# Kernel tuning notes

Hardware: AMD Instinct MI355X
Metric: run time of the kernel (lower is better)

## Reference

```python
import jax, jax.numpy as jnp
import numpy as np

D, E, H, B, K = 2, 16, 1024, 8192, 2  # depth, experts, width, tokens, selection_size


def setup_inputs() -> dict:
    key = jax.random.key(0)
    ks = jax.random.split(key, 6)
    X = jax.random.normal(ks[0], (B, H), dtype=jnp.float32)
    # gate Linear per layer (torch inits these to zero; small random used so top-k is nontrivial)
    gate_w = jax.random.normal(ks[1], (D, E, H), dtype=jnp.float32) * 0.02
    gate_b = jnp.zeros((D, E), dtype=jnp.float32)
    # per-expert Linear: weight [out,in], bias [out], stacked over (layer, expert)
    ew = jax.random.normal(ks[2], (D, E, H, H), dtype=jnp.float32) * (1.0 / np.float32(np.sqrt(H)))
    eb = jnp.zeros((D, E, H), dtype=jnp.float32)
    # PReLU params: left/right slopes ~ randn (as in torch init), position/bias zero
    pl = jax.random.normal(ks[3], (D, E, H), dtype=jnp.float32)
    pr = jax.random.normal(ks[4], (D, E, H), dtype=jnp.float32)
    pp = jnp.zeros((D, E, H), dtype=jnp.float32)
    pb = jnp.zeros((D, E, H), dtype=jnp.float32)
    return {"X": X, "gate_w": gate_w, "gate_b": gate_b, "ew": ew, "eb": eb,
            "pl": pl, "pr": pr, "pp": pp, "pb": pb}


def reference(X, gate_w, gate_b, ew, eb, pl, pr, pp, pb):
    x = X
    for d in range(D):  # small fixed layer loop
        # gating: Linear -> top-k -> softmax over selected logits
        G = jnp.einsum('bi,ei->be', x, gate_w[d]) + gate_b[d]          # [B,E]
        vals, idx = jax.lax.top_k(G, K)                                 # [B,K]
        w = jax.nn.softmax(vals, axis=-1)                               # [B,K]
        # expert Linear over all experts, then custom PReLU
        y = jnp.einsum('bi,eoi->beo', x, ew[d]) + eb[d]                 # [B,E,O]
        delta = y - pp[d]                                               # [B,E,O]
        act = pb[d] + jnp.where(delta >= 0, delta * pr[d], delta * pl[d])
        # gather selected experts and combine
        sel = jnp.take_along_axis(act, idx[:, :, None], axis=1)        # [B,K,O]
        x = jnp.einsum('bk,bko->bo', w, sel)                            # [B,O]
    return x
```

## Files before the change

### kernel.cpp

```cpp
#include <hip/hip_runtime.h>

#define H_ 1024
#define B_ 8192
#define E_ 16
#define D_ 2
#define BM 128
#define BN 128
#define BK 32
#define MAXT 144

typedef _Float16 f16;
typedef _Float16 f16x4 __attribute__((ext_vector_type(4)));
typedef _Float16 f16x8 __attribute__((ext_vector_type(8)));
typedef float    f32x4 __attribute__((ext_vector_type(4)));

__device__ __forceinline__ void gload16(const void* g, void* l) {
  __builtin_amdgcn_global_load_lds((const __attribute__((address_space(1))) void*)g,
                                   (__attribute__((address_space(3))) void*)l, 16, 0, 0);
}

__global__ void split_kernel(const float* __restrict__ s, f16* __restrict__ hp,
                             f16* __restrict__ lp, int n) {
  const int stride = gridDim.x * blockDim.x * 4;
  for (int i = (blockIdx.x * blockDim.x + threadIdx.x) * 4; i < n; i += stride) {
    float4 v = *(const float4*)(s + i);
    f16 h0 = (f16)v.x, h1 = (f16)v.y, h2 = (f16)v.z, h3 = (f16)v.w;
    f16 l0 = (f16)(v.x - (float)h0), l1 = (f16)(v.y - (float)h1);
    f16 l2 = (f16)(v.z - (float)h2), l3 = (f16)(v.w - (float)h3);
    *(f16x4*)(hp + i) = (f16x4){h0, h1, h2, h3};
    *(f16x4*)(lp + i) = (f16x4){l0, l1, l2, l3};
  }
}

__global__ void gate_split(const float* __restrict__ x, const float* __restrict__ gw,
                           const float* __restrict__ gb, f16* __restrict__ xh,
                           f16* __restrict__ xl, int2* __restrict__ tok_e,
                           float2* __restrict__ tok_w) {
  const int token = blockIdx.x * 4 + (threadIdx.x >> 6);
  const int lane = threadIdx.x & 63;
  const float4* xr = (const float4*)(x + (long)token * H_);
  f16x4* hr = (f16x4*)(xh + (long)token * H_);
  f16x4* lr = (f16x4*)(xl + (long)token * H_);
  float acc[E_];
#pragma unroll
  for (int e = 0; e < E_; ++e) acc[e] = 0.f;
#pragma unroll
  for (int i0 = 0; i0 < H_ / 4; i0 += 64) {
    float4 xv = xr[i0 + lane];
    f16 h0 = (f16)xv.x, h1 = (f16)xv.y, h2 = (f16)xv.z, h3 = (f16)xv.w;
    hr[i0 + lane] = (f16x4){h0, h1, h2, h3};
    lr[i0 + lane] = (f16x4){(f16)(xv.x - (float)h0), (f16)(xv.y - (float)h1),
                            (f16)(xv.z - (float)h2), (f16)(xv.w - (float)h3)};
#pragma unroll
    for (int e = 0; e < E_; ++e) {
      float4 gv = ((const float4*)(gw + e * H_))[i0 + lane];
      acc[e] = fmaf(xv.x, gv.x, fmaf(xv.y, gv.y, fmaf(xv.z, gv.z, fmaf(xv.w, gv.w, acc[e]))));
    }
  }
#pragma unroll
  for (int off = 32; off; off >>= 1) {
#pragma unroll
    for (int e = 0; e < E_; ++e) acc[e] += __shfl_xor(acc[e], off, 64);
  }
  if (lane == 0) {
    float g[E_];
#pragma unroll
    for (int e = 0; e < E_; ++e) g[e] = acc[e] + gb[e];
    int i0 = 0; float v0 = g[0];
#pragma unroll
    for (int e = 1; e < E_; ++e) if (g[e] > v0) { v0 = g[e]; i0 = e; }
    int i1 = -1; float v1 = -3.4e38f;
#pragma unroll
    for (int e = 0; e < E_; ++e) if (e != i0 && g[e] > v1) { v1 = g[e]; i1 = e; }
    float t = expf(v1 - v0);
    float s = 1.f / (1.f + t);
    tok_e[token] = (int2){i0, i1};
    tok_w[token] = (float2){s, t * s};
  }
}

__global__ void route_kernel(const int2* __restrict__ tok_e, const float2* __restrict__ tok_w,
                             int* __restrict__ lists, float* __restrict__ wlist,
                             int* __restrict__ counts) {
  __shared__ int cnt[E_];
  __shared__ int base[E_];
  const int tid = threadIdx.x;
  const int token = blockIdx.x * 256 + tid;
  if (tid < E_) cnt[tid] = 0;
  __syncthreads();
  int2 e = tok_e[token];
  float2 w = tok_w[token];
  int p0 = atomicAdd(&cnt[e.x], 1);
  int p1 = atomicAdd(&cnt[e.y], 1);
  __syncthreads();
  if (tid < E_) base[tid] = atomicAdd(&counts[tid], cnt[tid]);
  __syncthreads();
  int o0 = e.x * B_ + base[e.x] + p0;
  lists[o0] = token; wlist[o0] = w.x;
  int o1 = e.y * B_ + base[e.y] + p1;
  lists[o1] = token; wlist[o1] = w.y;
}

__global__ void build_tiles(const int* __restrict__ counts, int2* __restrict__ tiles,
                            int* __restrict__ ntile) {
  if (threadIdx.x == 0) {
    int n = 0;
    for (int e = 0; e < E_; ++e) {
      int c = counts[e];
      for (int mt = 0; mt * BM < c; ++mt) tiles[n++] = (int2){e, mt};
    }
    *ntile = n;
  }
}

__global__ __launch_bounds__(256, 4) void expert_gemm(
    const f16* __restrict__ xh, const f16* __restrict__ xl,
    const f16* __restrict__ wh, const f16* __restrict__ wl,
    const float* __restrict__ eb, const float* __restrict__ pl,
    const float* __restrict__ pr, const float* __restrict__ pp,
    const float* __restrict__ pb, const int* __restrict__ lists,
    const float* __restrict__ wlist, const int* __restrict__ counts,
    const int2* __restrict__ tiles, const int* __restrict__ ntile,
    float* __restrict__ out) {
  const int t = blockIdx.y;
  if (t >= *ntile) return;
  const int2 td = tiles[t];
  const int e = td.x, mt = td.y;
  const int cnt = counts[e];
  const int nt = blockIdx.x;

  __shared__ char smem[32768];

  const int tid = threadIdx.x;
  const int lane = tid & 63;
  const int wave = tid >> 6;
  const int wm = wave >> 1, wn = wave & 1;

  const int rl = lane >> 2;
  const int ks = ((lane & 3) - ((lane >> 3) & 3)) & 3;
  const int c0 = wave * 2, c1 = wave * 2 + 1;
  const int rA0 = c0 * 16 + rl, rA1 = c1 * 16 + rl;
  const int gr0 = mt * BM + rA0, gr1 = mt * BM + rA1;
  const int tok0 = (gr0 < cnt) ? lists[e * B_ + gr0] : 0;
  const int tok1 = (gr1 < cnt) ? lists[e * B_ + gr1] : 0;
  const long a0 = (long)tok0 * H_ + ks * 8;
  const long a1 = (long)tok1 * H_ + ks * 8;
  const long b0 = ((long)e * H_ + nt * BN + rA0) * H_ + ks * 8;
  const long b1 = ((long)e * H_ + nt * BN + rA1) * H_ + ks * 8;

  const int rm = lane & 15;
  const int sl = ((((lane >> 4) + (rm >> 1)) & 3) << 4);
  int offA[4], offB[4];
#pragma unroll
  for (int m = 0; m < 4; ++m) offA[m] = (wm * 64 + m * 16 + rm) * 64 + sl;
#pragma unroll
  for (int n = 0; n < 4; ++n) offB[n] = (wn * 64 + n * 16 + rm) * 64 + sl;

  f32x4 acc[4][4] = {};

  for (int kt = 0; kt < H_; kt += BK) {
    gload16(xh + a0 + kt, smem + c0 * 1024);
    gload16(xh + a1 + kt, smem + c1 * 1024);
    gload16(xl + a0 + kt, smem + 8192 + c0 * 1024);
    gload16(xl + a1 + kt, smem + 8192 + c1 * 1024);
    gload16(wh + b0 + kt, smem + 16384 + c0 * 1024);
    gload16(wh + b1 + kt, smem + 16384 + c1 * 1024);
    gload16(wl + b0 + kt, smem + 24576 + c0 * 1024);
    gload16(wl + b1 + kt, smem + 24576 + c1 * 1024);
    __syncthreads();

    f16x8 Amh[4], Aml[4], Bnh[4], Bnl[4];
#pragma unroll
    for (int m = 0; m < 4; ++m) {
      Amh[m] = *(const f16x8*)(smem + offA[m]);
      Aml[m] = *(const f16x8*)(smem + 8192 + offA[m]);
    }
#pragma unroll
    for (int n = 0; n < 4; ++n) {
      Bnh[n] = *(const f16x8*)(smem + 16384 + offB[n]);
      Bnl[n] = *(const f16x8*)(smem + 24576 + offB[n]);
    }
#pragma unroll
    for (int m = 0; m < 4; ++m) {
#pragma unroll
      for (int n = 0; n < 4; ++n) {
        acc[m][n] = __builtin_amdgcn_mfma_f32_16x16x32_f16(Amh[m], Bnh[n], acc[m][n], 0, 0, 0);
        acc[m][n] = __builtin_amdgcn_mfma_f32_16x16x32_f16(Amh[m], Bnl[n], acc[m][n], 0, 0, 0);
        acc[m][n] = __builtin_amdgcn_mfma_f32_16x16x32_f16(Aml[m], Bnh[n], acc[m][n], 0, 0, 0);
      }
    }
    __syncthreads();
  }

  float ebv[4], plv[4], prv[4], ppv[4], pbv[4];
  int Ocol[4];
#pragma unroll
  for (int n = 0; n < 4; ++n) {
    int O = nt * BN + wn * 64 + n * 16 + rm;
    Ocol[n] = O;
    int idx = e * H_ + O;
    ebv[n] = eb[idx]; plv[n] = pl[idx]; prv[n] = pr[idx]; ppv[n] = pp[idx]; pbv[n] = pb[idx];
  }
  const int rbase = (lane >> 4) * 4;
#pragma unroll
  for (int m = 0; m < 4; ++m) {
#pragma unroll
    for (int j = 0; j < 4; ++j) {
      int rloc = wm * 64 + m * 16 + rbase + j;
      int gr = mt * BM + rloc;
      if (gr < cnt) {
        float wgt = wlist[e * B_ + gr];
        long obase = (long)lists[e * B_ + gr] * H_;
#pragma unroll
        for (int n = 0; n < 4; ++n) {
          float y = acc[m][n][j] + ebv[n];
          float dlt = y - ppv[n];
          float act = pbv[n] + (dlt >= 0.f ? dlt * prv[n] : dlt * plv[n]);
          atomicAdd(out + obase + Ocol[n], wgt * act);
        }
      }
    }
  }
}

extern "C" void kernel_launch(void* const* d_in, const int* in_sizes, int n_in,
                              void* d_out, int out_size, void* d_ws, size_t ws_size,
                              hipStream_t stream) {
  const float* X  = (const float*)d_in[0];
  const float* GW = (const float*)d_in[1];
  const float* GB = (const float*)d_in[2];
  const float* EW = (const float*)d_in[3];
  const float* EB = (const float*)d_in[4];
  const float* PL = (const float*)d_in[5];
  const float* PR = (const float*)d_in[6];
  const float* PP = (const float*)d_in[7];
  const float* PB = (const float*)d_in[8];
  float* out = (float*)d_out;

  char* ws = (char*)d_ws;
  float* x1    = (float*)(ws);
  f16*   xh    = (f16*)(ws + 33554432);
  f16*   xl    = (f16*)(ws + 50331648);
  f16*   wh    = (f16*)(ws + 67108864);
  f16*   wl    = (f16*)(ws + 100663296);
  int*   lists = (int*)(ws + 134217728);
  float* wlist = (float*)(ws + 134742016);
  int*   counts= (int*)(ws + 135266304);
  int2*  tok_e = (int2*)(ws + 135266368);
  float2* tok_w= (float2*)(ws + 135331904);
  int2*  tiles = (int2*)(ws + 135397440);
  int*   ntile = (int*)(ws + 135398592);

  for (int d = 0; d < D_; ++d) {
    const float* xin = d ? x1 : X;
    float* xout = d ? out : x1;
    hipMemsetAsync(counts, 0, 64, stream);
    hipMemsetAsync(xout, 0, (size_t)B_ * H_ * 4, stream);
    split_kernel<<<2048, 256, 0, stream>>>(EW + (size_t)d * E_ * H_ * H_, wh, wl, E_ * H_ * H_);
    gate_split<<<B_ / 4, 256, 0, stream>>>(xin, GW + d * E_ * H_, GB + d * E_,
                                           xh, xl, tok_e, tok_w);
    route_kernel<<<B_ / 256, 256, 0, stream>>>(tok_e, tok_w, lists, wlist, counts);
    build_tiles<<<1, 64, 0, stream>>>(counts, tiles, ntile);
    expert_gemm<<<dim3(H_ / BN, MAXT), 256, 0, stream>>>(
        xh, xl, wh, wl, EB + d * E_ * H_, PL + d * E_ * H_, PR + d * E_ * H_,
        PP + d * E_ * H_, PB + d * E_ * H_, lists, wlist, counts, tiles, ntile, xout);
  }
}
```

Before: 643.7 us.

## Load GEMM operands directly from global into registers with double buffering

The expert GEMM no longer stages A and B tiles through LDS with barriers. Each lane now loads its MFMA fragments straight from global memory into registers, using two register sets so the loads for the next k-step overlap with the current MFMAs. Launch bounds drop to 2 blocks per SM to make room for the larger register footprint. The tile-list builder is also parallelised with a wave prefix scan. The risks are that lanes no longer share loaded data, so global and L2 traffic rises with uncoalesced per-lane 16-byte loads, and occupancy falls.

```diff
diff --git a/kernel.cpp b/kernel.cpp
--- a/kernel.cpp
+++ b/kernel.cpp
@@ -6,18 +6,12 @@
 #define D_ 2
 #define BM 128
 #define BN 128
-#define BK 32
 #define MAXT 144
 
 typedef _Float16 f16;
 typedef _Float16 f16x4 __attribute__((ext_vector_type(4)));
 typedef _Float16 f16x8 __attribute__((ext_vector_type(8)));
 typedef float    f32x4 __attribute__((ext_vector_type(4)));
-
-__device__ __forceinline__ void gload16(const void* g, void* l) {
-  __builtin_amdgcn_global_load_lds((const __attribute__((address_space(1))) void*)g,
-                                   (__attribute__((address_space(3))) void*)l, 16, 0, 0);
-}
 
 __global__ void split_kernel(const float* __restrict__ s, f16* __restrict__ hp,
                              f16* __restrict__ lp, int n) {
@@ -103,17 +97,23 @@
 
 __global__ void build_tiles(const int* __restrict__ counts, int2* __restrict__ tiles,
                             int* __restrict__ ntile) {
-  if (threadIdx.x == 0) {
-    int n = 0;
-    for (int e = 0; e < E_; ++e) {
-      int c = counts[e];
-      for (int mt = 0; mt * BM < c; ++mt) tiles[n++] = (int2){e, mt};
-    }
-    *ntile = n;
-  }
-}
-
-__global__ __launch_bounds__(256, 4) void expert_gemm(
+  const int lane = threadIdx.x;
+  int c = 0;
+  if (lane < E_) c = (counts[lane] + BM - 1) / BM;
+  int p = c;
+#pragma unroll
+  for (int off = 1; off < E_; off <<= 1) {
+    int v = __shfl_up(p, off, 64);
+    if (lane >= off) p += v;
+  }
+  if (lane == E_ - 1) *ntile = p;
+  int start = p - c;
+  if (lane < E_) {
+    for (int i = 0; i < c; ++i) tiles[start + i] = (int2){lane, i};
+  }
+}
+
+__global__ __launch_bounds__(256, 2) void expert_gemm(
     const f16* __restrict__ xh, const f16* __restrict__ xl,
     const f16* __restrict__ wh, const f16* __restrict__ wl,
     const float* __restrict__ eb, const float* __restrict__ pl,
@@ -129,68 +129,58 @@
   const int cnt = counts[e];
   const int nt = blockIdx.x;
 
-  __shared__ char smem[32768];
-
   const int tid = threadIdx.x;
   const int lane = tid & 63;
   const int wave = tid >> 6;
   const int wm = wave >> 1, wn = wave & 1;
-
-  const int rl = lane >> 2;
-  const int ks = ((lane & 3) - ((lane >> 3) & 3)) & 3;
-  const int c0 = wave * 2, c1 = wave * 2 + 1;
-  const int rA0 = c0 * 16 + rl, rA1 = c1 * 16 + rl;
-  const int gr0 = mt * BM + rA0, gr1 = mt * BM + rA1;
-  const int tok0 = (gr0 < cnt) ? lists[e * B_ + gr0] : 0;
-  const int tok1 = (gr1 < cnt) ? lists[e * B_ + gr1] : 0;
-  const long a0 = (long)tok0 * H_ + ks * 8;
-  const long a1 = (long)tok1 * H_ + ks * 8;
-  const long b0 = ((long)e * H_ + nt * BN + rA0) * H_ + ks * 8;
-  const long b1 = ((long)e * H_ + nt * BN + rA1) * H_ + ks * 8;
-
   const int rm = lane & 15;
-  const int sl = ((((lane >> 4) + (rm >> 1)) & 3) << 4);
-  int offA[4], offB[4];
-#pragma unroll
-  for (int m = 0; m < 4; ++m) offA[m] = (wm * 64 + m * 16 + rm) * 64 + sl;
-#pragma unroll
-  for (int n = 0; n < 4; ++n) offB[n] = (wn * 64 + n * 16 + rm) * 64 + sl;
+  const int koff = (lane >> 4) * 8;
+
+  long offA[4], offB[4];
+#pragma unroll
+  for (int m = 0; m < 4; ++m) {
+    int gr = mt * BM + wm * 64 + m * 16 + rm;
+    int tok = (gr < cnt) ? lists[e * B_ + gr] : 0;
+    offA[m] = (long)tok * H_ + koff;
+  }
+#pragma unroll
+  for (int n = 0; n < 4; ++n)
+    offB[n] = ((long)e * H_ + nt * BN + wn * 64 + n * 16 + rm) * H_ + koff;
 
   f32x4 acc[4][4] = {};
-
-  for (int kt = 0; kt < H_; kt += BK) {
-    gload16(xh + a0 + kt, smem + c0 * 1024);
-    gload16(xh + a1 + kt, smem + c1 * 1024);
-    gload16(xl + a0 + kt, smem + 8192 + c0 * 1024);
-    gload16(xl + a1 + kt, smem + 8192 + c1 * 1024);
-    gload16(wh + b0 + kt, smem + 16384 + c0 * 1024);
-    gload16(wh + b1 + kt, smem + 16384 + c1 * 1024);
-    gload16(wl + b0 + kt, smem + 24576 + c0 * 1024);
-    gload16(wl + b1 + kt, smem + 24576 + c1 * 1024);
-    __syncthreads();
-
-    f16x8 Amh[4], Aml[4], Bnh[4], Bnl[4];
-#pragma unroll
-    for (int m = 0; m < 4; ++m) {
-      Amh[m] = *(const f16x8*)(smem + offA[m]);
-      Aml[m] = *(const f16x8*)(smem + 8192 + offA[m]);
-    }
-#pragma unroll
-    for (int n = 0; n < 4; ++n) {
-      Bnh[n] = *(const f16x8*)(smem + 16384 + offB[n]);
-      Bnl[n] = *(const f16x8*)(smem + 24576 + offB[n]);
-    }
-#pragma unroll
-    for (int m = 0; m < 4; ++m) {
-#pragma unroll
-      for (int n = 0; n < 4; ++n) {
-        acc[m][n] = __builtin_amdgcn_mfma_f32_16x16x32_f16(Amh[m], Bnh[n], acc[m][n], 0, 0, 0);
-        acc[m][n] = __builtin_amdgcn_mfma_f32_16x16x32_f16(Amh[m], Bnl[n], acc[m][n], 0, 0, 0);
-        acc[m][n] = __builtin_amdgcn_mfma_f32_16x16x32_f16(Aml[m], Bnh[n], acc[m][n], 0, 0, 0);
-      }
-    }
-    __syncthreads();
-  }
+  f16x8 Ah0[4], Al0[4], Bh0[4], Bl0[4];
+  f16x8 Ah1[4], Al1[4], Bh1[4], Bl1[4];
+
+#define LOADSET(S, KT)                                          \
+  _Pragma("unroll") for (int m = 0; m < 4; ++m) {               \
+    Ah##S[m] = *(const f16x8*)(xh + offA[m] + (KT));            \
+    Al##S[m] = *(const f16x8*)(xl + offA[m] + (KT));            \
+  }                                                             \
+  _Pragma("unroll") for (int n = 0; n < 4; ++n) {               \
+    Bh##S[n] = *(const f16x8*)(wh + offB[n] + (KT));            \
+    Bl##S[n] = *(const f16x8*)(wl + offB[n] + (KT));            \
+  }
+
+#define MFMASET(S)                                                                             \
+  _Pragma("unroll") for (int m = 0; m < 4; ++m)                                                \
+  _Pragma("unroll") for (int n = 0; n < 4; ++n) {                                              \
+    acc[m][n] = __builtin_amdgcn_mfma_f32_16x16x32_f16(Ah##S[m], Bh##S[n], acc[m][n], 0, 0, 0);\
+    acc[m][n] = __builtin_amdgcn_mfma_f32_16x16x32_f16(Ah##S[m], Bl##S[n], acc[m][n], 0, 0, 0);\
+    acc[m][n] = __builtin_amdgcn_mfma_f32_16x16x32_f16(Al##S[m], Bh##S[n], acc[m][n], 0, 0, 0);\
+  }
+
+  LOADSET(0, 0)
+  LOADSET(1, 32)
+  for (int kt = 0; kt < H_ - 64; kt += 64) {
+    MFMASET(0)
+    LOADSET(0, kt + 64)
+    MFMASET(1)
+    LOADSET(1, kt + 96)
+  }
+  MFMASET(0)
+  MFMASET(1)
+#undef LOADSET
+#undef MFMASET
 
   float ebv[4], plv[4], prv[4], ppv[4], pbv[4];
   int Ocol[4];
```

Result: slower. 923.8 us (+43.5%).
